# Optimization experiments

Measured on AMD Instinct MI355X. Metric: run time of the kernel, lower is better.

The kernel has to match this reference:

```python
import jax, jax.numpy as jnp
import numpy as np
import math

B, Q_LEN, K_LEN = 8, 512, 512
D_MODEL, H = 512, 8
DK = D_MODEL // H


def setup_inputs() -> dict:
    key = jax.random.key(0)
    ks = jax.random.split(key, 12)
    inp = {
        "query": jax.random.normal(ks[0], (B, Q_LEN, D_MODEL), jnp.float32),
        "key": jax.random.normal(ks[1], (B, K_LEN, D_MODEL), jnp.float32),
        "value": jax.random.normal(ks[2], (B, K_LEN, D_MODEL), jnp.float32),
        "relative_embeddings": jax.random.normal(ks[3], (K_LEN, Q_LEN, D_MODEL), jnp.float32),
        # causal mask: 1 = attend, 0 = masked
        "mask": jnp.tril(jnp.ones((Q_LEN, K_LEN), dtype=bool)),
        "Wq": jax.random.normal(ks[4], (D_MODEL, D_MODEL), jnp.float32) / math.sqrt(D_MODEL),
        "Wk": jax.random.normal(ks[5], (D_MODEL, D_MODEL), jnp.float32) / math.sqrt(D_MODEL),
        "Wv": jax.random.normal(ks[6], (D_MODEL, D_MODEL), jnp.float32) / math.sqrt(D_MODEL),
        "Wo": jax.random.normal(ks[7], (D_MODEL, D_MODEL), jnp.float32) / math.sqrt(D_MODEL),
        "Wr": jax.random.normal(ks[8], (D_MODEL, D_MODEL), jnp.float32) / math.sqrt(D_MODEL),
        "u": jax.random.normal(ks[9], (H, DK), jnp.float32),
        "v": jax.random.normal(ks[10], (H, DK), jnp.float32),
    }
    return inp


def reference(query, key, value, relative_embeddings, mask, Wq, Wk, Wv, Wo, Wr, u, v):
    b, q_len, d_model = query.shape
    k_len = key.shape[1]
    # torch nn.Linear(x) = x @ W.T (bias=False)
    Qh = (query @ Wq.T).reshape(b, q_len, H, DK).transpose(0, 2, 1, 3)   # bhqd
    Kh = (key @ Wk.T).reshape(b, k_len, H, DK).transpose(0, 2, 1, 3)     # bhkd
    Vh = (value @ Wv.T).reshape(b, k_len, H, DK).transpose(0, 2, 1, 3)   # bhkd
    # relative position projection: (k_len, q_len, d_model)
    R = relative_embeddings @ Wr.T
    # view(k,q,H,dk).permute(2,1,0,3) -> (H, q, k, dk)
    Rh = R.reshape(k_len, q_len, H, DK).transpose(2, 1, 0, 3)
    # content score: (Q + u) K^T
    content = jnp.einsum("bhqd,bhkd->bhqk", Qh + u[None, :, None, :], Kh)
    # position score: (Q + v) R^T, R per-head per-query
    position = jnp.einsum("bhqd,hqkd->bhqk", Qh + v[None, :, None, :], Rh)
    scores = (content + position) / math.sqrt(DK)
    scores = jnp.where(mask[None, None, :, :], scores, -1e9)
    weights = jax.nn.softmax(scores, axis=-1)  # dropout is identity in eval
    out = jnp.einsum("bhqk,bhkd->bhqd", weights, Vh)
    out = out.transpose(0, 2, 1, 3).reshape(b, q_len, d_model)
    out = out @ Wo.T
    return (out, weights)
```

## Files before the change

kernel.cpp:

```cpp
#include <hip/hip_runtime.h>

#define BATCH   8
#define SEQ     512
#define DMODEL  512
#define NHEAD   8
#define DKH     64

typedef __attribute__((ext_vector_type(8))) short bf16x8;
typedef __attribute__((ext_vector_type(4))) float f32x4;

__device__ __forceinline__ short f2bf(float f) {
    union { float f; unsigned u; } v; v.f = f;
    unsigned r = v.u + 0x7FFFu + ((v.u >> 16) & 1u);
    return (short)(r >> 16);
}
__device__ __forceinline__ float bf2f(short s) {
    union { unsigned u; float f; } v; v.u = ((unsigned)(unsigned short)s) << 16;
    return v.f;
}

#define LDK 40

__device__ __forceinline__ void stage_f32(const float* __restrict__ base,
                                          int rstride, short* lds, int tid) {
    int r = tid >> 2, c = (tid & 3) << 3;
    const float* p = base + (size_t)r * rstride + c;
    float4 x = *(const float4*)p;
    float4 y = *(const float4*)(p + 4);
    union { short s[8]; bf16x8 v; } o;
    o.s[0] = f2bf(x.x); o.s[1] = f2bf(x.y); o.s[2] = f2bf(x.z); o.s[3] = f2bf(x.w);
    o.s[4] = f2bf(y.x); o.s[5] = f2bf(y.y); o.s[6] = f2bf(y.z); o.s[7] = f2bf(y.w);
    *(bf16x8*)(lds + r * LDK + c) = o.v;
}

__device__ __forceinline__ void stage_bf16(const short* __restrict__ base,
                                           int rstride, short* lds, int tid) {
    int r = tid >> 2, c = (tid & 3) << 3;
    bf16x8 v = *(const bf16x8*)(base + (size_t)r * rstride + c);
    *(bf16x8*)(lds + r * LDK + c) = v;
}

__device__ __forceinline__ void mma_tile(const short* As, const short* Bs,
                                         int lane, int wm, int wn, f32x4 acc[2][2]) {
    int lo = lane & 15, hi = lane >> 4;
    bf16x8 a0 = *(const bf16x8*)(As + (wm * 32 + lo) * LDK + hi * 8);
    bf16x8 a1 = *(const bf16x8*)(As + (wm * 32 + 16 + lo) * LDK + hi * 8);
    bf16x8 b0 = *(const bf16x8*)(Bs + (wn * 32 + lo) * LDK + hi * 8);
    bf16x8 b1 = *(const bf16x8*)(Bs + (wn * 32 + 16 + lo) * LDK + hi * 8);
    acc[0][0] = __builtin_amdgcn_mfma_f32_16x16x32_bf16(a0, b0, acc[0][0], 0, 0, 0);
    acc[0][1] = __builtin_amdgcn_mfma_f32_16x16x32_bf16(a0, b1, acc[0][1], 0, 0, 0);
    acc[1][0] = __builtin_amdgcn_mfma_f32_16x16x32_bf16(a1, b0, acc[1][0], 0, 0, 0);
    acc[1][1] = __builtin_amdgcn_mfma_f32_16x16x32_bf16(a1, b1, acc[1][1], 0, 0, 0);
}

__global__ __launch_bounds__(256) void qkvw_kernel(
        const float* __restrict__ query, const float* __restrict__ key_,
        const float* __restrict__ value,
        const float* __restrict__ Wq, const float* __restrict__ Wk,
        const float* __restrict__ Wv, const float* __restrict__ Wr,
        const float* __restrict__ uvec, const float* __restrict__ vvec,
        short* __restrict__ Qu, short* __restrict__ Qv,
        short* __restrict__ Kh, short* __restrict__ Vt,
        short* __restrict__ Wrt) {
    __shared__ short As[64 * LDK], Bs[64 * LDK];
    int f = blockIdx.x, tid = threadIdx.x;
    if (f >= 1536) {
        int base = (f - 1536) * 1024;
        #pragma unroll
        for (int j = 0; j < 4; j++) {
            int idx = base + j * 256 + tid;
            int n = idx >> 9, m = idx & 511;
            Wrt[idx] = f2bf(Wr[(size_t)m * 512 + n]);
        }
        return;
    }
    int i = f >> 3;
    int nt = i & 7;
    int gm = (f & 7) * 24 + (i >> 3);
    int mode = gm >> 6, mt = gm & 63;
    const float* x = mode == 0 ? query : (mode == 1 ? key_ : value);
    const float* W = mode == 0 ? Wq : (mode == 1 ? Wk : Wv);
    int lane = tid & 63, w = tid >> 6, wm = w >> 1, wn = w & 1;
    const float* Abase = x + (size_t)mt * 64 * DMODEL;
    const float* Bbase = W + (size_t)nt * 64 * DMODEL;
    f32x4 acc[2][2] = {};
    for (int kt = 0; kt < DMODEL; kt += 32) {
        __syncthreads();
        stage_f32(Abase + kt, DMODEL, As, tid);
        stage_f32(Bbase + kt, DMODEL, Bs, tid);
        __syncthreads();
        mma_tile(As, Bs, lane, wm, wn, acc);
    }
    int lo = lane & 15, hi = lane >> 4;
    for (int fm = 0; fm < 2; fm++)
        for (int fn = 0; fn < 2; fn++)
            for (int r = 0; r < 4; r++) {
                int m = mt * 64 + wm * 32 + fm * 16 + hi * 4 + r;
                int n = nt * 64 + wn * 32 + fn * 16 + lo;
                float val = acc[fm][fn][r];
                int b = m >> 9, s = m & 511, h = n >> 6, d = n & 63;
                if (mode == 0) {
                    size_t idx = ((size_t)(b * NHEAD + h) * SEQ + s) * DKH + d;
                    Qu[idx] = f2bf(val + uvec[n]);
                    Qv[idx] = f2bf(val + vvec[n]);
                } else if (mode == 1) {
                    Kh[((size_t)(b * NHEAD + h) * SEQ + s) * DKH + d] = f2bf(val);
                } else {
                    Vt[((size_t)(b * NHEAD + h) * DKH + d) * SEQ + s] = f2bf(val);
                }
            }
}

__global__ __launch_bounds__(256) void tc_kernel(const short* __restrict__ Qv,
                                                 const short* __restrict__ Wrt,
                                                 short* __restrict__ T2,
                                                 const short* __restrict__ Qu,
                                                 const short* __restrict__ Kh,
                                                 float* __restrict__ scores) {
    __shared__ short As[2 * 64 * LDK], Bs[2 * 64 * LDK];
    int f0 = blockIdx.x, tid = threadIdx.x;
    int lane = tid & 63, w = tid >> 6, wm = w >> 1, wn = w & 1;
    int lo = lane & 15, hi = lane >> 4;
    if (f0 < 512) {
        int x = f0 & 7, i = f0 >> 3;
        int mh = x * 64 + i;
        int mt = mh >> 3, h = mh & 7;
        int m0 = mt * 64, b = m0 >> 9, q0 = m0 & 511;
        int bh = b * NHEAD + h;
        const short* Abase = Qv + ((size_t)(b * NHEAD + h) * SEQ + q0) * DKH;
        stage_bf16(Abase + 0,  DKH, As,            tid);
        stage_bf16(Abase + 32, DKH, As + 64 * LDK, tid);
        __syncthreads();
        bf16x8 aq[2][2];
        #pragma unroll
        for (int ch = 0; ch < 2; ch++) {
            aq[ch][0] = *(const bf16x8*)(As + ch * 64 * LDK + (wm * 32 + lo) * LDK + hi * 8);
            aq[ch][1] = *(const bf16x8*)(As + ch * 64 * LDK + (wm * 32 + 16 + lo) * LDK + hi * 8);
        }
        for (int nt = 0; nt < 8; nt++) {
            const short* Bbase = Wrt + (size_t)nt * 64 * DMODEL + h * DKH;
            __syncthreads();
            stage_bf16(Bbase + 0,  DMODEL, Bs,            tid);
            stage_bf16(Bbase + 32, DMODEL, Bs + 64 * LDK, tid);
            __syncthreads();
            f32x4 acc[2][2] = {};
            #pragma unroll
            for (int ch = 0; ch < 2; ch++) {
                bf16x8 b0 = *(const bf16x8*)(Bs + ch * 64 * LDK + (wn * 32 + lo) * LDK + hi * 8);
                bf16x8 b1 = *(const bf16x8*)(Bs + ch * 64 * LDK + (wn * 32 + 16 + lo) * LDK + hi * 8);
                acc[0][0] = __builtin_amdgcn_mfma_f32_16x16x32_bf16(aq[ch][0], b0, acc[0][0], 0, 0, 0);
                acc[0][1] = __builtin_amdgcn_mfma_f32_16x16x32_bf16(aq[ch][0], b1, acc[0][1], 0, 0, 0);
                acc[1][0] = __builtin_amdgcn_mfma_f32_16x16x32_bf16(aq[ch][1], b0, acc[1][0], 0, 0, 0);
                acc[1][1] = __builtin_amdgcn_mfma_f32_16x16x32_bf16(aq[ch][1], b1, acc[1][1], 0, 0, 0);
            }
            for (int fm = 0; fm < 2; fm++)
                for (int fn = 0; fn < 2; fn++)
                    for (int r = 0; r < 4; r++) {
                        int q = q0 + wm * 32 + fm * 16 + hi * 4 + r;
                        int n = nt * 64 + wn * 32 + fn * 16 + lo;
                        T2[((size_t)q * 64 + bh) * DMODEL + n] = f2bf(acc[fm][fn][r]);
                    }
        }
    } else {
        int fi = f0 - 512;
        int x = fi & 7, i = fi >> 3;
        int bhl, qt;
        if (i < 32) { bhl = i >> 3;              qt = i & 7; }
        else        { bhl = 4 + ((i - 32) >> 3); qt = 7 - (i & 7); }
        int bh = x * 8 + bhl;
        const short* Abase = Qu + ((size_t)bh * SEQ + qt * 64) * DKH;
        stage_bf16(Abase + 0,  DKH, As,            tid);
        stage_bf16(Abase + 32, DKH, As + 64 * LDK, tid);
        __syncthreads();
        bf16x8 aq[2][2];
        #pragma unroll
        for (int ch = 0; ch < 2; ch++) {
            aq[ch][0] = *(const bf16x8*)(As + ch * 64 * LDK + (wm * 32 + lo) * LDK + hi * 8);
            aq[ch][1] = *(const bf16x8*)(As + ch * 64 * LDK + (wm * 32 + 16 + lo) * LDK + hi * 8);
        }
        for (int kt_ = 0; kt_ <= qt; kt_++) {
            const short* Bbase = Kh + ((size_t)bh * SEQ + kt_ * 64) * DKH;
            __syncthreads();
            stage_bf16(Bbase + 0,  DKH, Bs,            tid);
            stage_bf16(Bbase + 32, DKH, Bs + 64 * LDK, tid);
            __syncthreads();
            f32x4 acc[2][2] = {};
            #pragma unroll
            for (int ch = 0; ch < 2; ch++) {
                bf16x8 b0 = *(const bf16x8*)(Bs + ch * 64 * LDK + (wn * 32 + lo) * LDK + hi * 8);
                bf16x8 b1 = *(const bf16x8*)(Bs + ch * 64 * LDK + (wn * 32 + 16 + lo) * LDK + hi * 8);
                acc[0][0] = __builtin_amdgcn_mfma_f32_16x16x32_bf16(aq[ch][0], b0, acc[0][0], 0, 0, 0);
                acc[0][1] = __builtin_amdgcn_mfma_f32_16x16x32_bf16(aq[ch][0], b1, acc[0][1], 0, 0, 0);
                acc[1][0] = __builtin_amdgcn_mfma_f32_16x16x32_bf16(aq[ch][1], b0, acc[1][0], 0, 0, 0);
                acc[1][1] = __builtin_amdgcn_mfma_f32_16x16x32_bf16(aq[ch][1], b1, acc[1][1], 0, 0, 0);
            }
            for (int fm = 0; fm < 2; fm++)
                for (int fn = 0; fn < 2; fn++)
                    for (int r = 0; r < 4; r++) {
                        int q = qt * 64 + wm * 32 + fm * 16 + hi * 4 + r;
                        int k = kt_ * 64 + wn * 32 + fn * 16 + lo;
                        scores[((size_t)bh * SEQ + q) * SEQ + k] = acc[fm][fn][r];
                    }
        }
    }
}

__global__ __launch_bounds__(1024) void position_kernel(const short* __restrict__ T2,
                                                        const float* __restrict__ rel,
                                                        float* __restrict__ scores) {
    int bk = blockIdx.x;
    int x = bk & 7, idx = bk >> 3;
    int q = (idx < 32) ? (idx * 8 + x) : (511 - ((idx - 32) * 8 + x));
    __shared__ short Tl[64 * 512];
    int tid = threadIdx.x, w = tid >> 6, lane = tid & 63;
    const short* Tq = T2 + (size_t)q * (64 * DMODEL);
    #pragma unroll
    for (int it = 0; it < 4; ++it) {
        int chunk = it * 1024 + tid;
        int r = chunk >> 6, c = chunk & 63;
        bf16x8 v = *(const bf16x8*)(Tq + (size_t)chunk * 8);
        *(bf16x8*)(Tl + r * 512 + (c ^ (r & 7)) * 8) = v;
    }
    __syncthreads();
    int kbase = w * 32;
    if (kbase > q) return;
    int lo = lane & 15, hi = lane >> 4;
    const float* relq = rel + ((size_t)kbase * SEQ + q) * DMODEL;
    f32x4 acc[4][2] = {};
    for (int n = 0; n < DMODEL; n += 32) {
        bf16x8 a[4];
        #pragma unroll
        for (int fm = 0; fm < 4; fm++) {
            int rr = fm * 16 + lo;
            int g = ((n >> 3) + hi) ^ (rr & 7);
            a[fm] = *(const bf16x8*)(Tl + rr * 512 + g * 8);
        }
        bf16x8 bfrag[2];
        #pragma unroll
        for (int fk = 0; fk < 2; fk++) {
            const float* p = relq + (size_t)(fk * 16 + lo) * (SEQ * DMODEL) + n + hi * 8;
            float4 xv = *(const float4*)p;
            float4 yv = *(const float4*)(p + 4);
            union { short s[8]; bf16x8 v; } o;
            o.s[0] = f2bf(xv.x); o.s[1] = f2bf(xv.y); o.s[2] = f2bf(xv.z); o.s[3] = f2bf(xv.w);
            o.s[4] = f2bf(yv.x); o.s[5] = f2bf(yv.y); o.s[6] = f2bf(yv.z); o.s[7] = f2bf(yv.w);
            bfrag[fk] = o.v;
        }
        #pragma unroll
        for (int fm = 0; fm < 4; fm++) {
            acc[fm][0] = __builtin_amdgcn_mfma_f32_16x16x32_bf16(a[fm], bfrag[0], acc[fm][0], 0, 0, 0);
            acc[fm][1] = __builtin_amdgcn_mfma_f32_16x16x32_bf16(a[fm], bfrag[1], acc[fm][1], 0, 0, 0);
        }
    }
    #pragma unroll
    for (int fm = 0; fm < 4; fm++)
        #pragma unroll
        for (int fk = 0; fk < 2; fk++)
            #pragma unroll
            for (int r = 0; r < 4; r++) {
                int bh = fm * 16 + hi * 4 + r;
                int k = kbase + fk * 16 + lo;
                scores[((size_t)bh * SEQ + q) * SEQ + k] += acc[fm][fk][r];
            }
}

#define PSTR 520
__global__ __launch_bounds__(256) void pv_sm_kernel(float* __restrict__ scores,
                                                    const short* __restrict__ Vt,
                                                    short* __restrict__ attn) {
    __shared__ short Ps[64 * PSTR];
    __shared__ float invS_lds[64];
    int f = blockIdx.x;
    int i = f >> 3;
    int bhl, qt;
    if (i < 32) { bhl = i >> 3;            qt = i & 7; }
    else        { bhl = 4 + ((i - 32) >> 3); qt = 7 - (i & 7); }
    int bh = (f & 7) * 8 + bhl;
    int tid = threadIdx.x, lane = tid & 63, w = tid >> 6, wm = w >> 1, wn = w & 1;
    int kmax = (qt + 1) * 64;
    int r = tid >> 2, c4 = tid & 3;
    int q = qt * 64 + r;
    int cc = c4 * 8;
    float* row = scores + ((size_t)bh * SEQ + q) * SEQ;
    float S = 0.f;
    for (int kt = 0; kt < kmax; kt += 32) {
        float4 x = *(const float4*)(row + kt + cc);
        float4 y = *(const float4*)(row + kt + cc + 4);
        float p0 = (kt + cc + 0 <= q) ? __expf(x.x * 0.125f) : 0.f;
        float p1 = (kt + cc + 1 <= q) ? __expf(x.y * 0.125f) : 0.f;
        float p2 = (kt + cc + 2 <= q) ? __expf(x.z * 0.125f) : 0.f;
        float p3 = (kt + cc + 3 <= q) ? __expf(x.w * 0.125f) : 0.f;
        float p4 = (kt + cc + 4 <= q) ? __expf(y.x * 0.125f) : 0.f;
        float p5 = (kt + cc + 5 <= q) ? __expf(y.y * 0.125f) : 0.f;
        float p6 = (kt + cc + 6 <= q) ? __expf(y.z * 0.125f) : 0.f;
        float p7 = (kt + cc + 7 <= q) ? __expf(y.w * 0.125f) : 0.f;
        S += p0 + p1 + p2 + p3 + p4 + p5 + p6 + p7;
        union { short s[8]; bf16x8 v; } o;
        o.s[0] = f2bf(p0); o.s[1] = f2bf(p1); o.s[2] = f2bf(p2); o.s[3] = f2bf(p3);
        o.s[4] = f2bf(p4); o.s[5] = f2bf(p5); o.s[6] = f2bf(p6); o.s[7] = f2bf(p7);
        *(bf16x8*)(Ps + r * PSTR + kt + cc) = o.v;
    }
    S += __shfl_xor(S, 1); S += __shfl_xor(S, 2);
    float invS = 1.0f / S;
    if (c4 == 0) invS_lds[r] = invS;
    for (int kt = 0; kt < SEQ; kt += 32) {
        float4 o0, o1;
        if (kt < kmax) {
            const short* pr = Ps + r * PSTR + kt + cc;
            o0 = make_float4(bf2f(pr[0]) * invS, bf2f(pr[1]) * invS,
                             bf2f(pr[2]) * invS, bf2f(pr[3]) * invS);
            o1 = make_float4(bf2f(pr[4]) * invS, bf2f(pr[5]) * invS,
                             bf2f(pr[6]) * invS, bf2f(pr[7]) * invS);
        } else {
            o0 = make_float4(0.f, 0.f, 0.f, 0.f); o1 = o0;
        }
        *(float4*)(row + kt + cc) = o0;
        *(float4*)(row + kt + cc + 4) = o1;
    }
    __syncthreads();
    const short* Vtb = Vt + (size_t)bh * DKH * SEQ;
    int lo = lane & 15, hi = lane >> 4;
    f32x4 acc[2][2] = {};
    for (int kc = 0; kc < kmax; kc += 32) {
        bf16x8 a0 = *(const bf16x8*)(Ps + (wm * 32 + lo) * PSTR + kc + hi * 8);
        bf16x8 a1 = *(const bf16x8*)(Ps + (wm * 32 + 16 + lo) * PSTR + kc + hi * 8);
        bf16x8 b0 = *(const bf16x8*)(Vtb + (size_t)(wn * 32 + lo) * SEQ + kc + hi * 8);
        bf16x8 b1 = *(const bf16x8*)(Vtb + (size_t)(wn * 32 + 16 + lo) * SEQ + kc + hi * 8);
        acc[0][0] = __builtin_amdgcn_mfma_f32_16x16x32_bf16(a0, b0, acc[0][0], 0, 0, 0);
        acc[0][1] = __builtin_amdgcn_mfma_f32_16x16x32_bf16(a0, b1, acc[0][1], 0, 0, 0);
        acc[1][0] = __builtin_amdgcn_mfma_f32_16x16x32_bf16(a1, b0, acc[1][0], 0, 0, 0);
        acc[1][1] = __builtin_amdgcn_mfma_f32_16x16x32_bf16(a1, b1, acc[1][1], 0, 0, 0);
    }
    int b = bh >> 3, h = bh & 7;
    for (int fm = 0; fm < 2; fm++)
        for (int fn = 0; fn < 2; fn++)
            for (int rr = 0; rr < 4; rr++) {
                int ql = wm * 32 + fm * 16 + hi * 4 + rr;
                int d = wn * 32 + fn * 16 + lo;
                float val = acc[fm][fn][rr] * invS_lds[ql];
                attn[((size_t)b * SEQ + qt * 64 + ql) * DMODEL + h * DKH + d] = f2bf(val);
            }
}

__global__ __launch_bounds__(256) void oproj_kernel(const short* __restrict__ attn,
                                                    const float* __restrict__ Wo,
                                                    float* __restrict__ out) {
    __shared__ short As[64 * LDK], Bs[64 * LDK];
    int f = blockIdx.x;
    int i = f >> 3;
    int mt = (f & 7) * 8 + (i >> 3);
    int nt = i & 7;
    int tid = threadIdx.x, lane = tid & 63, w = tid >> 6, wm = w >> 1, wn = w & 1;
    const short* Abase = attn + (size_t)mt * 64 * DMODEL;
    const float* Bbase = Wo + (size_t)nt * 64 * DMODEL;
    f32x4 acc[2][2] = {};
    for (int kt = 0; kt < DMODEL; kt += 32) {
        __syncthreads();
        stage_bf16(Abase + kt, DMODEL, As, tid);
        stage_f32(Bbase + kt, DMODEL, Bs, tid);
        __syncthreads();
        mma_tile(As, Bs, lane, wm, wn, acc);
    }
    int lo = lane & 15, hi = lane >> 4;
    for (int fm = 0; fm < 2; fm++)
        for (int fn = 0; fn < 2; fn++)
            for (int r = 0; r < 4; r++) {
                int m = mt * 64 + wm * 32 + fm * 16 + hi * 4 + r;
                int n = nt * 64 + wn * 32 + fn * 16 + lo;
                out[(size_t)m * DMODEL + n] = acc[fm][fn][r];
            }
}

extern "C" void kernel_launch(void* const* d_in, const int* in_sizes, int n_in,
                              void* d_out, int out_size, void* d_ws, size_t ws_size,
                              hipStream_t stream) {
    (void)in_sizes; (void)n_in; (void)out_size; (void)ws_size;
    const float* query = (const float*)d_in[0];
    const float* key   = (const float*)d_in[1];
    const float* value = (const float*)d_in[2];
    const float* rel   = (const float*)d_in[3];
    const float* Wq = (const float*)d_in[5];
    const float* Wk = (const float*)d_in[6];
    const float* Wv = (const float*)d_in[7];
    const float* Wo = (const float*)d_in[8];
    const float* Wr = (const float*)d_in[9];
    const float* u  = (const float*)d_in[10];
    const float* v  = (const float*)d_in[11];

    float* out     = (float*)d_out;
    float* weights = out + (size_t)BATCH * SEQ * DMODEL;

    char* ws = (char*)d_ws;
    short* Qu   = (short*)(ws);
    short* Qv   = (short*)(ws + ((size_t)4 << 20));
    short* Kh   = (short*)(ws + ((size_t)8 << 20));
    short* Vt   = (short*)(ws + ((size_t)12 << 20));
    short* T2   = (short*)(ws + ((size_t)16 << 20));
    short* attn = (short*)(ws + ((size_t)48 << 20));
    short* Wrt  = (short*)(ws + ((size_t)52 << 20));

    qkvw_kernel<<<1792, 256, 0, stream>>>(query, key, value, Wq, Wk, Wv, Wr,
                                          u, v, Qu, Qv, Kh, Vt, Wrt);
    tc_kernel<<<1024, 256, 0, stream>>>(Qv, Wrt, T2, Qu, Kh, weights);
    position_kernel<<<512, 1024, 0, stream>>>(T2, rel, weights);
    pv_sm_kernel<<<512, 256, 0, stream>>>(weights, Vt, attn);
    oproj_kernel<<<512, 256, 0, stream>>>(attn, Wo, out);
}
```

Baseline: 193.1 us.

## Fuse softmax into position kernel, leaving PV kernel as plain matmul

Each position_kernel block covers one query row across all 64 batch-heads and every key, so the full softmax row is available there. The block now adds the content score, exponentiates, reduces row sums across waves through LDS, and writes normalized weights. This removes the separate read-exp-normalize-rewrite pass over the score matrix in the PV kernel, which now only converts weights to bf16 and multiplies by V. Idle waves in the masked region now stay resident until the block-wide barriers and write zeros instead of exiting early, which adds synchronization in the position kernel. Normalization is now applied before the bf16 conversion rather than after the PV accumulation.

```diff
diff --git a/kernel.cpp b/kernel.cpp
--- a/kernel.cpp
+++ b/kernel.cpp
@@ -13,10 +13,6 @@
     union { float f; unsigned u; } v; v.f = f;
     unsigned r = v.u + 0x7FFFu + ((v.u >> 16) & 1u);
     return (short)(r >> 16);
-}
-__device__ __forceinline__ float bf2f(short s) {
-    union { unsigned u; float f; } v; v.u = ((unsigned)(unsigned short)s) << 16;
-    return v.f;
 }
 
 #define LDK 40
@@ -212,6 +208,8 @@
     int x = bk & 7, idx = bk >> 3;
     int q = (idx < 32) ? (idx * 8 + x) : (511 - ((idx - 32) * 8 + x));
     __shared__ short Tl[64 * 512];
+    __shared__ float S_lds[16][64];
+    __shared__ float invS_lds[64];
     int tid = threadIdx.x, w = tid >> 6, lane = tid & 63;
     const short* Tq = T2 + (size_t)q * (64 * DMODEL);
     #pragma unroll
@@ -223,33 +221,35 @@
     }
     __syncthreads();
     int kbase = w * 32;
-    if (kbase > q) return;
-    int lo = lane & 15, hi = lane >> 4;
-    const float* relq = rel + ((size_t)kbase * SEQ + q) * DMODEL;
+    bool active = (kbase <= q);
+    int lo = lane & 15, hi = lane >> 4;
     f32x4 acc[4][2] = {};
-    for (int n = 0; n < DMODEL; n += 32) {
-        bf16x8 a[4];
-        #pragma unroll
-        for (int fm = 0; fm < 4; fm++) {
-            int rr = fm * 16 + lo;
-            int g = ((n >> 3) + hi) ^ (rr & 7);
-            a[fm] = *(const bf16x8*)(Tl + rr * 512 + g * 8);
-        }
-        bf16x8 bfrag[2];
-        #pragma unroll
-        for (int fk = 0; fk < 2; fk++) {
-            const float* p = relq + (size_t)(fk * 16 + lo) * (SEQ * DMODEL) + n + hi * 8;
-            float4 xv = *(const float4*)p;
-            float4 yv = *(const float4*)(p + 4);
-            union { short s[8]; bf16x8 v; } o;
-            o.s[0] = f2bf(xv.x); o.s[1] = f2bf(xv.y); o.s[2] = f2bf(xv.z); o.s[3] = f2bf(xv.w);
-            o.s[4] = f2bf(yv.x); o.s[5] = f2bf(yv.y); o.s[6] = f2bf(yv.z); o.s[7] = f2bf(yv.w);
-            bfrag[fk] = o.v;
-        }
-        #pragma unroll
-        for (int fm = 0; fm < 4; fm++) {
-            acc[fm][0] = __builtin_amdgcn_mfma_f32_16x16x32_bf16(a[fm], bfrag[0], acc[fm][0], 0, 0, 0);
-            acc[fm][1] = __builtin_amdgcn_mfma_f32_16x16x32_bf16(a[fm], bfrag[1], acc[fm][1], 0, 0, 0);
+    if (active) {
+        const float* relq = rel + ((size_t)kbase * SEQ + q) * DMODEL;
+        for (int n = 0; n < DMODEL; n += 32) {
+            bf16x8 a[4];
+            #pragma unroll
+            for (int fm = 0; fm < 4; fm++) {
+                int rr = fm * 16 + lo;
+                int g = ((n >> 3) + hi) ^ (rr & 7);
+                a[fm] = *(const bf16x8*)(Tl + rr * 512 + g * 8);
+            }
+            bf16x8 bfrag[2];
+            #pragma unroll
+            for (int fk = 0; fk < 2; fk++) {
+                const float* p = relq + (size_t)(fk * 16 + lo) * (SEQ * DMODEL) + n + hi * 8;
+                float4 xv = *(const float4*)p;
+                float4 yv = *(const float4*)(p + 4);
+                union { short s[8]; bf16x8 v; } o;
+                o.s[0] = f2bf(xv.x); o.s[1] = f2bf(xv.y); o.s[2] = f2bf(xv.z); o.s[3] = f2bf(xv.w);
+                o.s[4] = f2bf(yv.x); o.s[5] = f2bf(yv.y); o.s[6] = f2bf(yv.z); o.s[7] = f2bf(yv.w);
+                bfrag[fk] = o.v;
+            }
+            #pragma unroll
+            for (int fm = 0; fm < 4; fm++) {
+                acc[fm][0] = __builtin_amdgcn_mfma_f32_16x16x32_bf16(a[fm], bfrag[0], acc[fm][0], 0, 0, 0);
+                acc[fm][1] = __builtin_amdgcn_mfma_f32_16x16x32_bf16(a[fm], bfrag[1], acc[fm][1], 0, 0, 0);
+            }
         }
     }
     #pragma unroll
@@ -260,16 +260,47 @@
             for (int r = 0; r < 4; r++) {
                 int bh = fm * 16 + hi * 4 + r;
                 int k = kbase + fk * 16 + lo;
-                scores[((size_t)bh * SEQ + q) * SEQ + k] += acc[fm][fk][r];
+                float p = 0.f;
+                if (active && k <= q) {
+                    float c = scores[((size_t)bh * SEQ + q) * SEQ + k];
+                    p = __expf((acc[fm][fk][r] + c) * 0.125f);
+                }
+                acc[fm][fk][r] = p;
+            }
+    #pragma unroll
+    for (int fm = 0; fm < 4; fm++)
+        #pragma unroll
+        for (int r = 0; r < 4; r++) {
+            float s = acc[fm][0][r] + acc[fm][1][r];
+            s += __shfl_xor(s, 1); s += __shfl_xor(s, 2);
+            s += __shfl_xor(s, 4); s += __shfl_xor(s, 8);
+            if (lo == 0) S_lds[w][fm * 16 + hi * 4 + r] = s;
+        }
+    __syncthreads();
+    if (tid < 64) {
+        float s = 0.f;
+        #pragma unroll
+        for (int wv = 0; wv < 16; wv++) s += S_lds[wv][tid];
+        invS_lds[tid] = 1.0f / s;
+    }
+    __syncthreads();
+    #pragma unroll
+    for (int fm = 0; fm < 4; fm++)
+        #pragma unroll
+        for (int fk = 0; fk < 2; fk++)
+            #pragma unroll
+            for (int r = 0; r < 4; r++) {
+                int bh = fm * 16 + hi * 4 + r;
+                int k = kbase + fk * 16 + lo;
+                scores[((size_t)bh * SEQ + q) * SEQ + k] = acc[fm][fk][r] * invS_lds[bh];
             }
 }
 
 #define PSTR 520
-__global__ __launch_bounds__(256) void pv_sm_kernel(float* __restrict__ scores,
-                                                    const short* __restrict__ Vt,
-                                                    short* __restrict__ attn) {
+__global__ __launch_bounds__(256) void pv_kernel(const float* __restrict__ weights,
+                                                 const short* __restrict__ Vt,
+                                                 short* __restrict__ attn) {
     __shared__ short Ps[64 * PSTR];
-    __shared__ float invS_lds[64];
     int f = blockIdx.x;
     int i = f >> 3;
     int bhl, qt;
@@ -281,41 +312,14 @@
     int r = tid >> 2, c4 = tid & 3;
     int q = qt * 64 + r;
     int cc = c4 * 8;
-    float* row = scores + ((size_t)bh * SEQ + q) * SEQ;
-    float S = 0.f;
+    const float* row = weights + ((size_t)bh * SEQ + q) * SEQ;
     for (int kt = 0; kt < kmax; kt += 32) {
         float4 x = *(const float4*)(row + kt + cc);
         float4 y = *(const float4*)(row + kt + cc + 4);
-        float p0 = (kt + cc + 0 <= q) ? __expf(x.x * 0.125f) : 0.f;
-        float p1 = (kt + cc + 1 <= q) ? __expf(x.y * 0.125f) : 0.f;
-        float p2 = (kt + cc + 2 <= q) ? __expf(x.z * 0.125f) : 0.f;
-        float p3 = (kt + cc + 3 <= q) ? __expf(x.w * 0.125f) : 0.f;
-        float p4 = (kt + cc + 4 <= q) ? __expf(y.x * 0.125f) : 0.f;
-        float p5 = (kt + cc + 5 <= q) ? __expf(y.y * 0.125f) : 0.f;
-        float p6 = (kt + cc + 6 <= q) ? __expf(y.z * 0.125f) : 0.f;
-        float p7 = (kt + cc + 7 <= q) ? __expf(y.w * 0.125f) : 0.f;
-        S += p0 + p1 + p2 + p3 + p4 + p5 + p6 + p7;
         union { short s[8]; bf16x8 v; } o;
-        o.s[0] = f2bf(p0); o.s[1] = f2bf(p1); o.s[2] = f2bf(p2); o.s[3] = f2bf(p3);
-        o.s[4] = f2bf(p4); o.s[5] = f2bf(p5); o.s[6] = f2bf(p6); o.s[7] = f2bf(p7);
+        o.s[0] = f2bf(x.x); o.s[1] = f2bf(x.y); o.s[2] = f2bf(x.z); o.s[3] = f2bf(x.w);
+        o.s[4] = f2bf(y.x); o.s[5] = f2bf(y.y); o.s[6] = f2bf(y.z); o.s[7] = f2bf(y.w);
         *(bf16x8*)(Ps + r * PSTR + kt + cc) = o.v;
-    }
-    S += __shfl_xor(S, 1); S += __shfl_xor(S, 2);
-    float invS = 1.0f / S;
-    if (c4 == 0) invS_lds[r] = invS;
-    for (int kt = 0; kt < SEQ; kt += 32) {
-        float4 o0, o1;
-        if (kt < kmax) {
-            const short* pr = Ps + r * PSTR + kt + cc;
-            o0 = make_float4(bf2f(pr[0]) * invS, bf2f(pr[1]) * invS,
-                             bf2f(pr[2]) * invS, bf2f(pr[3]) * invS);
-            o1 = make_float4(bf2f(pr[4]) * invS, bf2f(pr[5]) * invS,
-                             bf2f(pr[6]) * invS, bf2f(pr[7]) * invS);
-        } else {
-            o0 = make_float4(0.f, 0.f, 0.f, 0.f); o1 = o0;
-        }
-        *(float4*)(row + kt + cc) = o0;
-        *(float4*)(row + kt + cc + 4) = o1;
     }
     __syncthreads();
     const short* Vtb = Vt + (size_t)bh * DKH * SEQ;
@@ -337,8 +341,7 @@
             for (int rr = 0; rr < 4; rr++) {
                 int ql = wm * 32 + fm * 16 + hi * 4 + rr;
                 int d = wn * 32 + fn * 16 + lo;
-                float val = acc[fm][fn][rr] * invS_lds[ql];
-                attn[((size_t)b * SEQ + qt * 64 + ql) * DMODEL + h * DKH + d] = f2bf(val);
+                attn[((size_t)b * SEQ + qt * 64 + ql) * DMODEL + h * DKH + d] = f2bf(acc[fm][fn][rr]);
             }
 }
 
@@ -403,6 +406,6 @@
                                           u, v, Qu, Qv, Kh, Vt, Wrt);
     tc_kernel<<<1024, 256, 0, stream>>>(Qv, Wrt, T2, Qu, Kh, weights);
     position_kernel<<<512, 1024, 0, stream>>>(T2, rel, weights);
-    pv_sm_kernel<<<512, 256, 0, stream>>>(weights, Vt, attn);
+    pv_kernel<<<512, 256, 0, stream>>>(weights, Vt, attn);
     oproj_kernel<<<512, 256, 0, stream>>>(attn, Wo, out);
 }
```

Result: no change. 196.4 us (+1.7%).
